# Kernel tuning notes

Measured on AMD Instinct MI355X. Metric: run time of the kernel, lower is better.

## Reference

```python
import jax, jax.numpy as jnp
import numpy as np

N = 30000      # nodes
E = 480000     # edges (before self loops)
DIN = 128      # dim_in
DH = 32        # dim_h (per-head out channels)
H1 = 8         # gat1 heads
H2 = 2         # gat2 heads
G = 64         # num graphs in batch
DOUT = 10      # dim_out
NEG_SLOPE = 0.2


def _glorot(key, shape):
    fan_in = shape[0]
    return jax.random.normal(key, shape, dtype=jnp.float32) / np.sqrt(fan_in)


def setup_inputs() -> dict:
    key = jax.random.key(0)
    ks = jax.random.split(key, 16)
    x = jax.random.normal(ks[0], (N, DIN), dtype=jnp.float32)
    edge_index = jax.random.randint(ks[1], (2, E), 0, N, dtype=jnp.int32)
    batch = jnp.sort(jax.random.randint(ks[2], (N,), 0, G, dtype=jnp.int32))
    # GATv2Conv layer 1: lin_l, lin_r (dim_in -> H1*DH), att (H1, DH), bias (H1*DH)
    W1l = _glorot(ks[3], (DIN, H1 * DH))
    W1r = _glorot(ks[4], (DIN, H1 * DH))
    a1 = _glorot(ks[5], (DH, H1)).T  # [H1, DH]
    b1 = jnp.zeros((H1 * DH,), dtype=jnp.float32)
    # GATv2Conv layer 2: (H1*DH -> H2*DH)
    W2l = _glorot(ks[6], (H1 * DH, H2 * DH))
    W2r = _glorot(ks[7], (H1 * DH, H2 * DH))
    a2 = _glorot(ks[8], (DH, H2)).T  # [H2, DH]
    b2 = jnp.zeros((H2 * DH,), dtype=jnp.float32)
    # MLP head: fc1(2*DH -> DH), fc2(DH -> DH//2), fc(DH//2 -> DOUT); stored [in,out]
    fc1_w = _glorot(ks[9], (2 * DH, DH)); fc1_b = jnp.zeros((DH,), jnp.float32)
    fc2_w = _glorot(ks[10], (DH, DH // 2)); fc2_b = jnp.zeros((DH // 2,), jnp.float32)
    fc_w = _glorot(ks[11], (DH // 2, DOUT)); fc_b = jnp.zeros((DOUT,), jnp.float32)
    return {"x": x, "edge_index": edge_index, "batch": batch,
            "W1l": W1l, "W1r": W1r, "a1": a1, "b1": b1,
            "W2l": W2l, "W2r": W2r, "a2": a2, "b2": b2,
            "fc1_w": fc1_w, "fc1_b": fc1_b, "fc2_w": fc2_w, "fc2_b": fc2_b,
            "fc_w": fc_w, "fc_b": fc_b}


def gatv2_conv(x, edge_index, Wl, Wr, att, bias, heads, dh, n):
    """PyG GATv2Conv: concat=True, add_self_loops=True, negative_slope=0.2."""
    src, dst = edge_index[0], edge_index[1]
    loop = jnp.arange(n, dtype=src.dtype)        # self loops (PyG default)
    src = jnp.concatenate([src, loop])
    dst = jnp.concatenate([dst, loop])
    xl = (x @ Wl).reshape(n, heads, dh)          # source transform
    xr = (x @ Wr).reshape(n, heads, dh)          # destination transform
    xj = xl[src]                                  # [Etot, H, dh] message features
    s = jax.nn.leaky_relu(xj + xr[dst], NEG_SLOPE)
    e = jnp.einsum('ehd,hd->eh', s, att)          # per-edge per-head score
    # segment softmax over incoming edges of each destination node
    m = jax.ops.segment_max(e, dst, num_segments=n)
    p = jnp.exp(e - m[dst])
    z = jax.ops.segment_sum(p, dst, num_segments=n)
    alpha = p / z[dst]                            # [Etot, H]
    out = jax.ops.segment_sum(xj * alpha[..., None], dst, num_segments=n)
    return out.reshape(n, heads * dh) + bias


def reference(x, edge_index, batch, W1l, W1r, a1, b1, W2l, W2r, a2, b2,
              fc1_w, fc1_b, fc2_w, fc2_b, fc_w, fc_b):
    h = gatv2_conv(x, edge_index, W1l, W1r, a1, b1, H1, DH, N)
    h = jax.nn.elu(h)
    h = gatv2_conv(h, edge_index, W2l, W2r, a2, b2, H2, DH, N)  # [N, 2*DH]
    # global_mean_pool
    sums = jax.ops.segment_sum(h, batch, num_segments=G)
    cnt = jax.ops.segment_sum(jnp.ones((N,), h.dtype), batch, num_segments=G)
    hg = sums / jnp.maximum(cnt, 1.0)[:, None]    # [G, 2*DH]
    x1 = jax.nn.relu(hg @ fc1_w + fc1_b)
    # dropout p=0.2 is identity in eval mode
    x2 = jax.nn.relu(x1 @ fc2_w + fc2_b)
    c = x2 @ fc_w + fc_b
    return (c, x2)
```

## Files before the change

kernel.cpp:

```cpp
#include <hip/hip_runtime.h>
#include <math.h>

#define DIN 128
#define DH  32
#define H1  8
#define H2  2
#define GNUM 64
#define DOUT 10
#define NEG_SLOPE 0.2f
#define SCAN_B 512

typedef __attribute__((ext_vector_type(8))) short sv8;
typedef __attribute__((ext_vector_type(4))) short sv4;
typedef __attribute__((ext_vector_type(4))) float fv4;

static __device__ __forceinline__ unsigned short f2bf(float f) {
    unsigned int u = __float_as_uint(f);
    unsigned int r = (u + 0x7fffu + ((u >> 16) & 1u)) >> 16;
    return (unsigned short)r;
}
static __device__ __forceinline__ float bf2f(unsigned short h) {
    return __uint_as_float(((unsigned int)h) << 16);
}

__global__ void k_deg(const int* __restrict__ dst, int* __restrict__ deg, int E, int n) {
    int i = blockIdx.x * blockDim.x + threadIdx.x;
    if (i < E) {
        atomicAdd(&deg[dst[i]], 1);
    } else if (i < E + n) {
        atomicAdd(&deg[i - E], 1);
    }
}

__global__ __launch_bounds__(SCAN_B)
void k_scan_partial(const int* __restrict__ deg, int* __restrict__ bsum, int n) {
    int i = blockIdx.x * SCAN_B + threadIdx.x;
    int v = (i < n) ? deg[i] : 0;
    #pragma unroll
    for (int m = 32; m >= 1; m >>= 1) v += __shfl_xor(v, m);
    __shared__ int red[SCAN_B / 64];
    if ((threadIdx.x & 63) == 0) red[threadIdx.x >> 6] = v;
    __syncthreads();
    if (threadIdx.x == 0) {
        int s = 0;
        #pragma unroll
        for (int k = 0; k < SCAN_B / 64; ++k) s += red[k];
        bsum[blockIdx.x] = s;
    }
}

__global__ __launch_bounds__(SCAN_B)
void k_scan_apply(int* __restrict__ deg, int* __restrict__ cursor,
                  const int* __restrict__ bsum, int n, int nb) {
    __shared__ int buf[SCAN_B];
    __shared__ int pfx_s, tot_s;
    const int t = threadIdx.x, b = blockIdx.x;
    if (t < 64) {
        int v = (t < nb) ? bsum[t] : 0;
        int incl = v;
        #pragma unroll
        for (int o = 1; o < 64; o <<= 1) {
            int w = __shfl_up(incl, o);
            if (t >= o) incl += w;
        }
        int pfx = (b == 0) ? 0 : __shfl(incl, b - 1);
        int tot = __shfl(incl, nb - 1);
        if (t == 0) { pfx_s = pfx; tot_s = tot; }
    }
    int i = b * SCAN_B + t;
    int v = (i < n) ? deg[i] : 0;
    buf[t] = v;
    __syncthreads();
    for (int o = 1; o < SCAN_B; o <<= 1) {
        int a = (t >= o) ? buf[t - o] : 0;
        __syncthreads();
        buf[t] += a;
        __syncthreads();
    }
    int excl = buf[t] - v + pfx_s;
    if (i < n) { deg[i] = excl; cursor[i] = excl; }
    if (b == 0 && t == 0) deg[n] = tot_s;
}

__global__ void k_scatter(const int* __restrict__ src, const int* __restrict__ dst,
                          int* __restrict__ cursor, int* __restrict__ csr_src, int E, int n) {
    int i = blockIdx.x * blockDim.x + threadIdx.x;
    if (i < E) {
        int d = dst[i];
        int pos = atomicAdd(&cursor[d], 1);
        csr_src[pos] = src[i];
    } else if (i < E + n) {
        int v = i - E;
        int pos = atomicAdd(&cursor[v], 1);
        csr_src[pos] = v;
    }
}

__global__ void k_prep(const float* __restrict__ W1l, const float* __restrict__ W1r,
                       const float* __restrict__ W2l, const float* __restrict__ W2r,
                       short* __restrict__ B1th, short* __restrict__ B1tl,
                       short* __restrict__ B2th, short* __restrict__ B2tl) {
    int id = blockIdx.x * blockDim.x + threadIdx.x;
    const int T1 = 512 * 128;
    const int T2 = 128 * 256;
    if (id < T1) {
        int n = id / 128, k = id - n * 128;
        float v = (n < 256) ? W1l[(size_t)k * 256 + n] : W1r[(size_t)k * 256 + (n - 256)];
        unsigned short h = f2bf(v);
        B1th[id] = (short)h;
        B1tl[id] = (short)f2bf(v - bf2f(h));
    } else if (id < T1 + T2) {
        int id2 = id - T1;
        int n = id2 / 256, k = id2 - n * 256;
        float v = (n < 64) ? W2l[(size_t)k * 64 + n] : W2r[(size_t)k * 64 + (n - 64)];
        unsigned short h = f2bf(v);
        B2th[id2] = (short)h;
        B2tl[id2] = (short)f2bf(v - bf2f(h));
    }
}

__global__ __launch_bounds__(256)
void k_gemm_mfma(const float* __restrict__ A, const short* __restrict__ Bth,
                 const short* __restrict__ Btl,
                 unsigned short* __restrict__ Cl, float* __restrict__ Cr,
                 int M, int K, int Ntot, int NL) {
    __shared__ union {
        struct { short hi[128 * 40]; short lo[128 * 40]; } a;
        float c[64 * 132];
    } sm;
    const int tid = threadIdx.x;
    const int lane = tid & 63;
    const int wid = tid >> 6;
    const int wm = wid & 1, wn = wid >> 1;
    const int m0 = blockIdx.x * 128;
    const int n0 = blockIdx.y * 128;
    const int l15 = lane & 15, q = lane >> 4;

    fv4 acc[4][4] = {};

    for (int kk = 0; kk < K; kk += 32) {
        __syncthreads();
        #pragma unroll
        for (int i = 0; i < 4; ++i) {
            int idx = tid + i * 256;
            int row = idx >> 3;
            int qq  = idx & 7;
            int mg  = m0 + row;
            float4 v = make_float4(0.f, 0.f, 0.f, 0.f);
            if (mg < M) v = *(const float4*)(A + (size_t)mg * K + kk + qq * 4);
            unsigned short hx = f2bf(v.x), hy = f2bf(v.y), hz = f2bf(v.z), hw = f2bf(v.w);
            sv4 hi = { (short)hx, (short)hy, (short)hz, (short)hw };
            sv4 lo = { (short)f2bf(v.x - bf2f(hx)), (short)f2bf(v.y - bf2f(hy)),
                       (short)f2bf(v.z - bf2f(hz)), (short)f2bf(v.w - bf2f(hw)) };
            *(sv4*)&sm.a.hi[row * 40 + qq * 4] = hi;
            *(sv4*)&sm.a.lo[row * 40 + qq * 4] = lo;
        }
        __syncthreads();

        sv8 bh[4], bl[4];
        #pragma unroll
        for (int fn = 0; fn < 4; ++fn) {
            int ng = n0 + wn * 64 + fn * 16 + l15;
            bh[fn] = *(const sv8*)(Bth + (size_t)ng * K + kk + q * 8);
            bl[fn] = *(const sv8*)(Btl + (size_t)ng * K + kk + q * 8);
        }
        #pragma unroll
        for (int fm = 0; fm < 4; ++fm) {
            int rl = wm * 64 + fm * 16 + l15;
            sv8 ah = *(const sv8*)&sm.a.hi[rl * 40 + q * 8];
            sv8 al = *(const sv8*)&sm.a.lo[rl * 40 + q * 8];
            #pragma unroll
            for (int fn = 0; fn < 4; ++fn) {
                acc[fm][fn] = __builtin_amdgcn_mfma_f32_16x16x32_bf16(ah, bh[fn], acc[fm][fn], 0, 0, 0);
                acc[fm][fn] = __builtin_amdgcn_mfma_f32_16x16x32_bf16(ah, bl[fn], acc[fm][fn], 0, 0, 0);
                acc[fm][fn] = __builtin_amdgcn_mfma_f32_16x16x32_bf16(al, bh[fn], acc[fm][fn], 0, 0, 0);
            }
        }
    }

    const int NR = Ntot - NL;
    #pragma unroll
    for (int s = 0; s < 2; ++s) {
        __syncthreads();
        if (wm == s) {
            #pragma unroll
            for (int fm = 0; fm < 4; ++fm)
                #pragma unroll
                for (int fn = 0; fn < 4; ++fn)
                    #pragma unroll
                    for (int r = 0; r < 4; ++r)
                        sm.c[(fm * 16 + q * 4 + r) * 132 + wn * 64 + fn * 16 + l15] = acc[fm][fn][r];
        }
        __syncthreads();
        #pragma unroll
        for (int i = 0; i < 2; ++i) {
            int lr = (tid >> 3) + i * 32;
            int grow = m0 + s * 64 + lr;
            if (grow < M) {
                #pragma unroll
                for (int k4 = 0; k4 < 4; ++k4) {
                    int jj = (tid & 7) + k4 * 8;
                    float4 vv = *(float4*)&sm.c[lr * 132 + jj * 4];
                    int gcol = n0 + jj * 4;
                    if (gcol < NL) {
                        ushort4 uu;
                        uu.x = f2bf(vv.x); uu.y = f2bf(vv.y);
                        uu.z = f2bf(vv.z); uu.w = f2bf(vv.w);
                        *(ushort4*)(Cl + (size_t)grow * NL + gcol) = uu;
                    } else {
                        *(float4*)(Cr + (size_t)grow * NR + (gcol - NL)) = vv;
                    }
                }
            }
        }
    }
}

__global__ __launch_bounds__(256)
void k_gemm_mfma_bf(const unsigned short* __restrict__ A, const short* __restrict__ Bth,
                    const short* __restrict__ Btl,
                    unsigned short* __restrict__ Cl, float* __restrict__ Cr,
                    int M, int K, int Ntot, int NL) {
    __shared__ union {
        short a[128 * 40];
        float c[64 * 132];
    } sm;
    const int tid = threadIdx.x;
    const int lane = tid & 63;
    const int wid = tid >> 6;
    const int wm = wid & 1, wn = wid >> 1;
    const int m0 = blockIdx.x * 128;
    const int n0 = blockIdx.y * 128;
    const int l15 = lane & 15, q = lane >> 4;

    fv4 acc[4][4] = {};

    for (int kk = 0; kk < K; kk += 32) {
        __syncthreads();
        #pragma unroll
        for (int i = 0; i < 2; ++i) {
            int idx = tid + i * 256;
            int row = idx >> 2;
            int qq  = idx & 3;
            int mg  = m0 + row;
            sv8 v = { 0, 0, 0, 0, 0, 0, 0, 0 };
            if (mg < M) v = *(const sv8*)(A + (size_t)mg * K + kk + qq * 8);
            *(sv8*)&sm.a[row * 40 + qq * 8] = v;
        }
        __syncthreads();

        sv8 bh[4], bl[4];
        #pragma unroll
        for (int fn = 0; fn < 4; ++fn) {
            int ng = n0 + wn * 64 + fn * 16 + l15;
            bh[fn] = *(const sv8*)(Bth + (size_t)ng * K + kk + q * 8);
            bl[fn] = *(const sv8*)(Btl + (size_t)ng * K + kk + q * 8);
        }
        #pragma unroll
        for (int fm = 0; fm < 4; ++fm) {
            int rl = wm * 64 + fm * 16 + l15;
            sv8 ah = *(const sv8*)&sm.a[rl * 40 + q * 8];
            #pragma unroll
            for (int fn = 0; fn < 4; ++fn) {
                acc[fm][fn] = __builtin_amdgcn_mfma_f32_16x16x32_bf16(ah, bh[fn], acc[fm][fn], 0, 0, 0);
                acc[fm][fn] = __builtin_amdgcn_mfma_f32_16x16x32_bf16(ah, bl[fn], acc[fm][fn], 0, 0, 0);
            }
        }
    }

    const int NR = Ntot - NL;
    #pragma unroll
    for (int s = 0; s < 2; ++s) {
        __syncthreads();
        if (wm == s) {
            #pragma unroll
            for (int fm = 0; fm < 4; ++fm)
                #pragma unroll
                for (int fn = 0; fn < 4; ++fn)
                    #pragma unroll
                    for (int r = 0; r < 4; ++r)
                        sm.c[(fm * 16 + q * 4 + r) * 132 + wn * 64 + fn * 16 + l15] = acc[fm][fn][r];
        }
        __syncthreads();
        #pragma unroll
        for (int i = 0; i < 2; ++i) {
            int lr = (tid >> 3) + i * 32;
            int grow = m0 + s * 64 + lr;
            if (grow < M) {
                #pragma unroll
                for (int k4 = 0; k4 < 4; ++k4) {
                    int jj = (tid & 7) + k4 * 8;
                    float4 vv = *(float4*)&sm.c[lr * 132 + jj * 4];
                    int gcol = n0 + jj * 4;
                    if (gcol < NL) {
                        ushort4 uu;
                        uu.x = f2bf(vv.x); uu.y = f2bf(vv.y);
                        uu.z = f2bf(vv.z); uu.w = f2bf(vv.w);
                        *(ushort4*)(Cl + (size_t)grow * NL + gcol) = uu;
                    } else {
                        *(float4*)(Cr + (size_t)grow * NR + (gcol - NL)) = vv;
                    }
                }
            }
        }
    }
}

static __device__ __forceinline__ void edge_acc(const float4 xl, const float4 xr,
                                                const float4 av, float& z, float4& acc) {
    float tx = xl.x + xr.x, ty = xl.y + xr.y, tz = xl.z + xr.z, tw = xl.w + xr.w;
    float lx = fmaxf(tx, 0.f) + NEG_SLOPE * fminf(tx, 0.f);
    float ly = fmaxf(ty, 0.f) + NEG_SLOPE * fminf(ty, 0.f);
    float lz = fmaxf(tz, 0.f) + NEG_SLOPE * fminf(tz, 0.f);
    float lw = fmaxf(tw, 0.f) + NEG_SLOPE * fminf(tw, 0.f);
    float s = lx * av.x + ly * av.y + lz * av.z + lw * av.w;
    s += __shfl_xor(s, 1);
    s += __shfl_xor(s, 2);
    s += __shfl_xor(s, 4);
    float w = __expf(s);
    z += w;
    acc.x = fmaf(w, xl.x, acc.x);
    acc.y = fmaf(w, xl.y, acc.y);
    acc.z = fmaf(w, xl.z, acc.z);
    acc.w = fmaf(w, xl.w, acc.w);
}

static __device__ __forceinline__ float4 bfx4(const ushort4 u) {
    float4 f;
    f.x = bf2f(u.x); f.y = bf2f(u.y); f.z = bf2f(u.z); f.w = bf2f(u.w);
    return f;
}

__global__ __launch_bounds__(256)
void k_edge1(const unsigned short* __restrict__ XLB, const float* __restrict__ XR,
             const int* __restrict__ offs, const int* __restrict__ csr,
             const float* __restrict__ att, const float* __restrict__ bias,
             unsigned short* __restrict__ out, int n) {
    const int lane = threadIdx.x & 63;
    const int wid  = threadIdx.x >> 6;
    const int v = blockIdx.x * 4 + wid;
    if (v >= n) return;
    const float4 xr = *(const float4*)(XR + (size_t)v * 256 + lane * 4);
    const float4 av = *(const float4*)(att + lane * 4);
    const float4 bv = *(const float4*)(bias + lane * 4);
    float z = 0.f;
    float4 acc = make_float4(0.f, 0.f, 0.f, 0.f);
    const int e0 = offs[v], e1 = offs[v + 1];
    int j = e0;
    for (; j + 4 <= e1; j += 4) {
        int s0 = csr[j], s1 = csr[j + 1], s2 = csr[j + 2], s3 = csr[j + 3];
        ushort4 u0 = *(const ushort4*)(XLB + (size_t)s0 * 256 + lane * 4);
        ushort4 u1 = *(const ushort4*)(XLB + (size_t)s1 * 256 + lane * 4);
        ushort4 u2 = *(const ushort4*)(XLB + (size_t)s2 * 256 + lane * 4);
        ushort4 u3 = *(const ushort4*)(XLB + (size_t)s3 * 256 + lane * 4);
        edge_acc(bfx4(u0), xr, av, z, acc);
        edge_acc(bfx4(u1), xr, av, z, acc);
        edge_acc(bfx4(u2), xr, av, z, acc);
        edge_acc(bfx4(u3), xr, av, z, acc);
    }
    for (; j < e1; ++j) {
        int s0 = csr[j];
        ushort4 u0 = *(const ushort4*)(XLB + (size_t)s0 * 256 + lane * 4);
        edge_acc(bfx4(u0), xr, av, z, acc);
    }
    const float rz = 1.f / z;
    float4 o;
    o.x = fmaf(acc.x, rz, bv.x);
    o.y = fmaf(acc.y, rz, bv.y);
    o.z = fmaf(acc.z, rz, bv.z);
    o.w = fmaf(acc.w, rz, bv.w);
    o.x = (o.x > 0.f) ? o.x : (__expf(o.x) - 1.f);
    o.y = (o.y > 0.f) ? o.y : (__expf(o.y) - 1.f);
    o.z = (o.z > 0.f) ? o.z : (__expf(o.z) - 1.f);
    o.w = (o.w > 0.f) ? o.w : (__expf(o.w) - 1.f);
    ushort4 hv;
    hv.x = f2bf(o.x); hv.y = f2bf(o.y); hv.z = f2bf(o.z); hv.w = f2bf(o.w);
    *(ushort4*)(out + (size_t)v * 256 + lane * 4) = hv;
}

__global__ __launch_bounds__(256)
void k_edge2(const unsigned short* __restrict__ XLB, const float* __restrict__ XR,
             const int* __restrict__ offs, const int* __restrict__ csr,
             const float* __restrict__ att, const float* __restrict__ bias,
             float* __restrict__ out, int n) {
    const int lane = threadIdx.x & 63;
    const int wid  = threadIdx.x >> 6;
    const int v = blockIdx.x * 4 + wid;
    if (v >= n) return;
    const int grp = lane >> 4, li = lane & 15;
    const float4 xr = *(const float4*)(XR + (size_t)v * 64 + li * 4);
    const float4 av = *(const float4*)(att + li * 4);
    float z = 0.f;
    float4 acc = make_float4(0.f, 0.f, 0.f, 0.f);
    const int e0 = offs[v], e1 = offs[v + 1];
    for (int j0 = e0; j0 < e1; j0 += 4) {
        const int j = j0 + grp;
        const bool valid = (j < e1);
        const int src = valid ? csr[j] : v;
        ushort4 u = *(const ushort4*)(XLB + (size_t)src * 64 + li * 4);
        float4 xl = bfx4(u);
        float tx = xl.x + xr.x, ty = xl.y + xr.y, tz = xl.z + xr.z, tw = xl.w + xr.w;
        float lx = fmaxf(tx, 0.f) + NEG_SLOPE * fminf(tx, 0.f);
        float ly = fmaxf(ty, 0.f) + NEG_SLOPE * fminf(ty, 0.f);
        float lz = fmaxf(tz, 0.f) + NEG_SLOPE * fminf(tz, 0.f);
        float lw = fmaxf(tw, 0.f) + NEG_SLOPE * fminf(tw, 0.f);
        float s = lx * av.x + ly * av.y + lz * av.z + lw * av.w;
        s += __shfl_xor(s, 1);
        s += __shfl_xor(s, 2);
        s += __shfl_xor(s, 4);
        float w = valid ? __expf(s) : 0.f;
        z += w;
        acc.x = fmaf(w, xl.x, acc.x);
        acc.y = fmaf(w, xl.y, acc.y);
        acc.z = fmaf(w, xl.z, acc.z);
        acc.w = fmaf(w, xl.w, acc.w);
    }
    z += __shfl_xor(z, 16); z += __shfl_xor(z, 32);
    acc.x += __shfl_xor(acc.x, 16); acc.x += __shfl_xor(acc.x, 32);
    acc.y += __shfl_xor(acc.y, 16); acc.y += __shfl_xor(acc.y, 32);
    acc.z += __shfl_xor(acc.z, 16); acc.z += __shfl_xor(acc.z, 32);
    acc.w += __shfl_xor(acc.w, 16); acc.w += __shfl_xor(acc.w, 32);
    if (grp == 0) {
        const float4 bv = *(const float4*)(bias + li * 4);
        const float rz = 1.f / z;
        float4 o;
        o.x = fmaf(acc.x, rz, bv.x);
        o.y = fmaf(acc.y, rz, bv.y);
        o.z = fmaf(acc.z, rz, bv.z);
        o.w = fmaf(acc.w, rz, bv.w);
        *(float4*)(out + (size_t)v * 64 + li * 4) = o;
    }
}

__global__ __launch_bounds__(256)
void k_pool_mlp(const float* __restrict__ out2, const int* __restrict__ batch,
                const float* __restrict__ fc1w, const float* __restrict__ fc1b,
                const float* __restrict__ fc2w, const float* __restrict__ fc2b,
                const float* __restrict__ fcw,  const float* __restrict__ fcb,
                float* __restrict__ outc, float* __restrict__ outx2, int n) {
    const int g = blockIdx.x;
    const int t = threadIdx.x;
    const int lane = t & 63;
    const int w = t >> 6;
    __shared__ float red[4][64];
    __shared__ float hg_s[64];
    __shared__ float x1_s[32];
    __shared__ float x2_s[16];

    int lo = 0, hi = n;
    while (lo < hi) { int mid = (lo + hi) >> 1; if (batch[mid] < g) lo = mid + 1; else hi = mid; }
    const int start = lo;
    hi = n;
    while (lo < hi) { int mid = (lo + hi) >> 1; if (batch[mid] < g + 1) lo = mid + 1; else hi = mid; }
    const int end = lo;

    float s = 0.f;
    for (int v = start + w; v < end; v += 4)
        s += out2[(size_t)v * 64 + lane];
    red[w][lane] = s;
    __syncthreads();
    if (w == 0) {
        float tot = red[0][lane] + red[1][lane] + red[2][lane] + red[3][lane];
        float cnt = fmaxf((float)(end - start), 1.0f);
        hg_s[lane] = tot / cnt;
    }
    __syncthreads();
    if (t < 32) {
        float a = fc1b[t];
        #pragma unroll
        for (int k = 0; k < 64; ++k) a = fmaf(hg_s[k], fc1w[k * 32 + t], a);
        x1_s[t] = fmaxf(a, 0.f);
    }
    __syncthreads();
    if (t < 16) {
        float a = fc2b[t];
        #pragma unroll
        for (int k = 0; k < 32; ++k) a = fmaf(x1_s[k], fc2w[k * 16 + t], a);
        x2_s[t] = fmaxf(a, 0.f);
    }
    __syncthreads();
    if (t < DOUT) {
        float a = fcb[t];
        #pragma unroll
        for (int k = 0; k < 16; ++k) a = fmaf(x2_s[k], fcw[k * 10 + t], a);
        outc[g * DOUT + t] = a;
    }
    if (t < 16) outx2[g * 16 + t] = x2_s[t];
}

extern "C" void kernel_launch(void* const* d_in, const int* in_sizes, int n_in,
                              void* d_out, int out_size, void* d_ws, size_t ws_size,
                              hipStream_t stream) {
    const float* x    = (const float*)d_in[0];
    const int*   ei   = (const int*)d_in[1];
    const int*   batch= (const int*)d_in[2];
    const float* W1l  = (const float*)d_in[3];
    const float* W1r  = (const float*)d_in[4];
    const float* a1   = (const float*)d_in[5];
    const float* b1   = (const float*)d_in[6];
    const float* W2l  = (const float*)d_in[7];
    const float* W2r  = (const float*)d_in[8];
    const float* a2   = (const float*)d_in[9];
    const float* b2   = (const float*)d_in[10];
    const float* fc1w = (const float*)d_in[11];
    const float* fc1b = (const float*)d_in[12];
    const float* fc2w = (const float*)d_in[13];
    const float* fc2b = (const float*)d_in[14];
    const float* fcw  = (const float*)d_in[15];
    const float* fcb  = (const float*)d_in[16];

    const int N = in_sizes[2];
    const int E = in_sizes[1] / 2;
    const int ET = E + N;
    const int* esrc = ei;
    const int* edst = ei + E;
    const int NB = (N + SCAN_B - 1) / SCAN_B;

    char* ws = (char*)d_ws;
    size_t off = 0;
    unsigned short* xl1b = (unsigned short*)(ws + off);  off += (size_t)N * 256 * 2;
    float* xr1  = (float*)(ws + off);            off += (size_t)N * 256 * 4;
    unsigned short* h1b = (unsigned short*)(ws + off);   off += (size_t)N * 256 * 2;
    int*   deg   = (int*)(ws + off);             off += ((size_t)(N + 1) * 4 + 255) & ~255ull;
    int*   cursor= (int*)(ws + off);             off += ((size_t)N * 4 + 255) & ~255ull;
    int*   csr   = (int*)(ws + off);             off += ((size_t)ET * 4 + 255) & ~255ull;
    int*   bsum  = (int*)(ws + off);             off += ((size_t)(NB + 1) * 4 + 255) & ~255ull;
    short* B1th  = (short*)(ws + off);           off += (size_t)512 * 128 * 2;
    short* B1tl  = (short*)(ws + off);           off += (size_t)512 * 128 * 2;
    short* B2th  = (short*)(ws + off);           off += (size_t)128 * 256 * 2;
    short* B2tl  = (short*)(ws + off);           off += (size_t)128 * 256 * 2;
    unsigned short* xl2b = xl1b;
    float* xr2  = xr1;
    float* out2 = xr1 + (size_t)N * 64;
    (void)ws_size; (void)n_in; (void)out_size;

    float* outc  = (float*)d_out;
    float* outx2 = (float*)d_out + GNUM * DOUT;

    hipMemsetAsync(deg, 0, (size_t)(N + 1) * 4, stream);

    int tb = 256;
    int gb = (ET + tb - 1) / tb;
    k_deg<<<gb, tb, 0, stream>>>(edst, deg, E, N);
    k_scan_partial<<<NB, SCAN_B, 0, stream>>>(deg, bsum, N);
    k_scan_apply<<<NB, SCAN_B, 0, stream>>>(deg, cursor, bsum, N, NB);
    k_scatter<<<gb, tb, 0, stream>>>(esrc, edst, cursor, csr, E, N);

    k_prep<<<(512 * 128 + 128 * 256 + 255) / 256, 256, 0, stream>>>(
        W1l, W1r, W2l, W2r, B1th, B1tl, B2th, B2tl);

    dim3 g1((N + 127) / 128, 4);
    k_gemm_mfma<<<g1, 256, 0, stream>>>(x, B1th, B1tl, xl1b, xr1, N, DIN, 512, 256);

    k_edge1<<<(N + 3) / 4, 256, 0, stream>>>(xl1b, xr1, deg, csr, a1, b1, h1b, N);

    dim3 g2((N + 127) / 128, 1);
    k_gemm_mfma_bf<<<g2, 256, 0, stream>>>(h1b, B2th, B2tl, xl2b, xr2, N, 256, 128, 64);

    k_edge2<<<(N + 3) / 4, 256, 0, stream>>>(xl2b, xr2, deg, csr, a2, b2, out2, N);

    k_pool_mlp<<<GNUM, 256, 0, stream>>>(out2, batch, fc1w, fc1b, fc2w, fc2b,
                                         fcw, fcb, outc, outx2, N);
}
```

Before: 317.5 us.

## Use persistent atomic work queues for edge kernels and pre-split x to bf16

The two edge-aggregation kernels become persistent: a fixed grid of 2048 blocks where each wavefront takes destination nodes from an atomic counter, aiming for better load balance across skewed node degrees. LeakyReLU inside the attention score is rewritten as 0.6*t + 0.4*|t|, and bf16 unpacking now uses bit masks on uint2 loads. The input x is split into bf16 hi/lo arrays once in the prep kernel, so the first GEMM loads pre-split data instead of converting it in each of its four column blocks. The degree memset is folded into the prep kernel, which also zeros the queue counters. This adds a full extra write and read pass over x and one atomic per node in exchange.

```diff
diff --git a/kernel.cpp b/kernel.cpp
--- a/kernel.cpp
+++ b/kernel.cpp
@@ -23,84 +23,15 @@
     return __uint_as_float(((unsigned int)h) << 16);
 }
 
-__global__ void k_deg(const int* __restrict__ dst, int* __restrict__ deg, int E, int n) {
-    int i = blockIdx.x * blockDim.x + threadIdx.x;
-    if (i < E) {
-        atomicAdd(&deg[dst[i]], 1);
-    } else if (i < E + n) {
-        atomicAdd(&deg[i - E], 1);
-    }
-}
-
-__global__ __launch_bounds__(SCAN_B)
-void k_scan_partial(const int* __restrict__ deg, int* __restrict__ bsum, int n) {
-    int i = blockIdx.x * SCAN_B + threadIdx.x;
-    int v = (i < n) ? deg[i] : 0;
-    #pragma unroll
-    for (int m = 32; m >= 1; m >>= 1) v += __shfl_xor(v, m);
-    __shared__ int red[SCAN_B / 64];
-    if ((threadIdx.x & 63) == 0) red[threadIdx.x >> 6] = v;
-    __syncthreads();
-    if (threadIdx.x == 0) {
-        int s = 0;
-        #pragma unroll
-        for (int k = 0; k < SCAN_B / 64; ++k) s += red[k];
-        bsum[blockIdx.x] = s;
-    }
-}
-
-__global__ __launch_bounds__(SCAN_B)
-void k_scan_apply(int* __restrict__ deg, int* __restrict__ cursor,
-                  const int* __restrict__ bsum, int n, int nb) {
-    __shared__ int buf[SCAN_B];
-    __shared__ int pfx_s, tot_s;
-    const int t = threadIdx.x, b = blockIdx.x;
-    if (t < 64) {
-        int v = (t < nb) ? bsum[t] : 0;
-        int incl = v;
-        #pragma unroll
-        for (int o = 1; o < 64; o <<= 1) {
-            int w = __shfl_up(incl, o);
-            if (t >= o) incl += w;
-        }
-        int pfx = (b == 0) ? 0 : __shfl(incl, b - 1);
-        int tot = __shfl(incl, nb - 1);
-        if (t == 0) { pfx_s = pfx; tot_s = tot; }
-    }
-    int i = b * SCAN_B + t;
-    int v = (i < n) ? deg[i] : 0;
-    buf[t] = v;
-    __syncthreads();
-    for (int o = 1; o < SCAN_B; o <<= 1) {
-        int a = (t >= o) ? buf[t - o] : 0;
-        __syncthreads();
-        buf[t] += a;
-        __syncthreads();
-    }
-    int excl = buf[t] - v + pfx_s;
-    if (i < n) { deg[i] = excl; cursor[i] = excl; }
-    if (b == 0 && t == 0) deg[n] = tot_s;
-}
-
-__global__ void k_scatter(const int* __restrict__ src, const int* __restrict__ dst,
-                          int* __restrict__ cursor, int* __restrict__ csr_src, int E, int n) {
-    int i = blockIdx.x * blockDim.x + threadIdx.x;
-    if (i < E) {
-        int d = dst[i];
-        int pos = atomicAdd(&cursor[d], 1);
-        csr_src[pos] = src[i];
-    } else if (i < E + n) {
-        int v = i - E;
-        int pos = atomicAdd(&cursor[v], 1);
-        csr_src[pos] = v;
-    }
-}
-
-__global__ void k_prep(const float* __restrict__ W1l, const float* __restrict__ W1r,
+__global__ void k_prep(const float* __restrict__ x,
+                       const float* __restrict__ W1l, const float* __restrict__ W1r,
                        const float* __restrict__ W2l, const float* __restrict__ W2r,
                        short* __restrict__ B1th, short* __restrict__ B1tl,
-                       short* __restrict__ B2th, short* __restrict__ B2tl) {
+                       short* __restrict__ B2th, short* __restrict__ B2tl,
+                       unsigned short* __restrict__ Xh, unsigned short* __restrict__ Xl,
+                       int* __restrict__ deg, int nz, int NK) {
     int id = blockIdx.x * blockDim.x + threadIdx.x;
+    if (id < nz) deg[id] = 0;
     const int T1 = 512 * 128;
     const int T2 = 128 * 256;
     if (id < T1) {
@@ -116,14 +47,93 @@
         unsigned short h = f2bf(v);
         B2th[id2] = (short)h;
         B2tl[id2] = (short)f2bf(v - bf2f(h));
+    } else if (id < T1 + T2 + NK) {
+        int e = id - T1 - T2;
+        float v = x[e];
+        unsigned short h = f2bf(v);
+        Xh[e] = h;
+        Xl[e] = f2bf(v - bf2f(h));
+    }
+}
+
+__global__ void k_deg(const int* __restrict__ dst, int* __restrict__ deg, int E, int n) {
+    int i = blockIdx.x * blockDim.x + threadIdx.x;
+    if (i < E) {
+        atomicAdd(&deg[dst[i]], 1);
+    } else if (i < E + n) {
+        atomicAdd(&deg[i - E], 1);
+    }
+}
+
+__global__ __launch_bounds__(SCAN_B)
+void k_scan_partial(const int* __restrict__ deg, int* __restrict__ bsum, int n) {
+    int i = blockIdx.x * SCAN_B + threadIdx.x;
+    int v = (i < n) ? deg[i] : 0;
+    #pragma unroll
+    for (int m = 32; m >= 1; m >>= 1) v += __shfl_xor(v, m);
+    __shared__ int red[SCAN_B / 64];
+    if ((threadIdx.x & 63) == 0) red[threadIdx.x >> 6] = v;
+    __syncthreads();
+    if (threadIdx.x == 0) {
+        int s = 0;
+        #pragma unroll
+        for (int k = 0; k < SCAN_B / 64; ++k) s += red[k];
+        bsum[blockIdx.x] = s;
+    }
+}
+
+__global__ __launch_bounds__(SCAN_B)
+void k_scan_apply(int* __restrict__ deg, int* __restrict__ cursor,
+                  const int* __restrict__ bsum, int n, int nb) {
+    __shared__ int buf[SCAN_B];
+    __shared__ int pfx_s, tot_s;
+    const int t = threadIdx.x, b = blockIdx.x;
+    if (t < 64) {
+        int v = (t < nb) ? bsum[t] : 0;
+        int incl = v;
+        #pragma unroll
+        for (int o = 1; o < 64; o <<= 1) {
+            int w = __shfl_up(incl, o);
+            if (t >= o) incl += w;
+        }
+        int pfx = (b == 0) ? 0 : __shfl(incl, b - 1);
+        int tot = __shfl(incl, nb - 1);
+        if (t == 0) { pfx_s = pfx; tot_s = tot; }
+    }
+    int i = b * SCAN_B + t;
+    int v = (i < n) ? deg[i] : 0;
+    buf[t] = v;
+    __syncthreads();
+    for (int o = 1; o < SCAN_B; o <<= 1) {
+        int a = (t >= o) ? buf[t - o] : 0;
+        __syncthreads();
+        buf[t] += a;
+        __syncthreads();
+    }
+    int excl = buf[t] - v + pfx_s;
+    if (i < n) { deg[i] = excl; cursor[i] = excl; }
+    if (b == 0 && t == 0) deg[n] = tot_s;
+}
+
+__global__ void k_scatter(const int* __restrict__ src, const int* __restrict__ dst,
+                          int* __restrict__ cursor, int* __restrict__ csr_src, int E, int n) {
+    int i = blockIdx.x * blockDim.x + threadIdx.x;
+    if (i < E) {
+        int d = dst[i];
+        int pos = atomicAdd(&cursor[d], 1);
+        csr_src[pos] = src[i];
+    } else if (i < E + n) {
+        int v = i - E;
+        int pos = atomicAdd(&cursor[v], 1);
+        csr_src[pos] = v;
     }
 }
 
 __global__ __launch_bounds__(256)
-void k_gemm_mfma(const float* __restrict__ A, const short* __restrict__ Bth,
-                 const short* __restrict__ Btl,
-                 unsigned short* __restrict__ Cl, float* __restrict__ Cr,
-                 int M, int K, int Ntot, int NL) {
+void k_gemm_split(const unsigned short* __restrict__ Ah, const unsigned short* __restrict__ Al,
+                  const short* __restrict__ Bth, const short* __restrict__ Btl,
+                  unsigned short* __restrict__ Cl, float* __restrict__ Cr,
+                  int M, int K, int Ntot, int NL) {
     __shared__ union {
         struct { short hi[128 * 40]; short lo[128 * 40]; } a;
         float c[64 * 132];
@@ -143,17 +153,15 @@
         #pragma unroll
         for (int i = 0; i < 4; ++i) {
             int idx = tid + i * 256;
-            int row = idx >> 3;
-            int qq  = idx & 7;
-            int mg  = m0 + row;
-            float4 v = make_float4(0.f, 0.f, 0.f, 0.f);
-            if (mg < M) v = *(const float4*)(A + (size_t)mg * K + kk + qq * 4);
-            unsigned short hx = f2bf(v.x), hy = f2bf(v.y), hz = f2bf(v.z), hw = f2bf(v.w);
-            sv4 hi = { (short)hx, (short)hy, (short)hz, (short)hw };
-            sv4 lo = { (short)f2bf(v.x - bf2f(hx)), (short)f2bf(v.y - bf2f(hy)),
-                       (short)f2bf(v.z - bf2f(hz)), (short)f2bf(v.w - bf2f(hw)) };
-            *(sv4*)&sm.a.hi[row * 40 + qq * 4] = hi;
-            *(sv4*)&sm.a.lo[row * 40 + qq * 4] = lo;
+            int arr = idx >> 9;
+            int c = idx & 511;
+            int row = c >> 2, qq = c & 3;
+            int mg = m0 + row;
+            const unsigned short* srcp = arr ? Al : Ah;
+            sv8 v = { 0, 0, 0, 0, 0, 0, 0, 0 };
+            if (mg < M) v = *(const sv8*)(srcp + (size_t)mg * K + kk + qq * 8);
+            short* dst = arr ? sm.a.lo : sm.a.hi;
+            *(sv8*)&dst[row * 40 + qq * 8] = v;
         }
         __syncthreads();
 
@@ -217,10 +225,10 @@
 }
 
 __global__ __launch_bounds__(256)
-void k_gemm_mfma_bf(const unsigned short* __restrict__ A, const short* __restrict__ Bth,
-                    const short* __restrict__ Btl,
-                    unsigned short* __restrict__ Cl, float* __restrict__ Cr,
-                    int M, int K, int Ntot, int NL) {
+void k_gemm_bf(const unsigned short* __restrict__ A, const short* __restrict__ Bth,
+               const short* __restrict__ Btl,
+               unsigned short* __restrict__ Cl, float* __restrict__ Cr,
+               int M, int K, int Ntot, int NL) {
     __shared__ union {
         short a[128 * 40];
         float c[64 * 132];
@@ -240,9 +248,8 @@
         #pragma unroll
         for (int i = 0; i < 2; ++i) {
             int idx = tid + i * 256;
-            int row = idx >> 2;
-            int qq  = idx & 3;
-            int mg  = m0 + row;
+            int row = idx >> 2, qq = idx & 3;
+            int mg = m0 + row;
             sv8 v = { 0, 0, 0, 0, 0, 0, 0, 0 };
             if (mg < M) v = *(const sv8*)(A + (size_t)mg * K + kk + qq * 8);
             *(sv8*)&sm.a[row * 40 + qq * 8] = v;
@@ -306,129 +313,145 @@
     }
 }
 
-static __device__ __forceinline__ void edge_acc(const float4 xl, const float4 xr,
+static __device__ __forceinline__ void edge_acc(const uint2 w, const float4 xr,
                                                 const float4 av, float& z, float4& acc) {
-    float tx = xl.x + xr.x, ty = xl.y + xr.y, tz = xl.z + xr.z, tw = xl.w + xr.w;
-    float lx = fmaxf(tx, 0.f) + NEG_SLOPE * fminf(tx, 0.f);
-    float ly = fmaxf(ty, 0.f) + NEG_SLOPE * fminf(ty, 0.f);
-    float lz = fmaxf(tz, 0.f) + NEG_SLOPE * fminf(tz, 0.f);
-    float lw = fmaxf(tw, 0.f) + NEG_SLOPE * fminf(tw, 0.f);
-    float s = lx * av.x + ly * av.y + lz * av.z + lw * av.w;
+    float fx = __uint_as_float(w.x << 16);
+    float fy = __uint_as_float(w.x & 0xffff0000u);
+    float fz = __uint_as_float(w.y << 16);
+    float fw = __uint_as_float(w.y & 0xffff0000u);
+    float tx = fx + xr.x, ty = fy + xr.y, tz = fz + xr.z, tw = fw + xr.w;
+    float s1 = tx * av.x;
+    s1 = fmaf(ty, av.y, s1);
+    s1 = fmaf(tz, av.z, s1);
+    s1 = fmaf(tw, av.w, s1);
+    float s2 = fabsf(tx) * av.x;
+    s2 = fmaf(fabsf(ty), av.y, s2);
+    s2 = fmaf(fabsf(tz), av.z, s2);
+    s2 = fmaf(fabsf(tw), av.w, s2);
+    float s = fmaf(0.6f, s1, 0.4f * s2);
     s += __shfl_xor(s, 1);
     s += __shfl_xor(s, 2);
     s += __shfl_xor(s, 4);
-    float w = __expf(s);
-    z += w;
-    acc.x = fmaf(w, xl.x, acc.x);
-    acc.y = fmaf(w, xl.y, acc.y);
-    acc.z = fmaf(w, xl.z, acc.z);
-    acc.w = fmaf(w, xl.w, acc.w);
-}
-
-static __device__ __forceinline__ float4 bfx4(const ushort4 u) {
-    float4 f;
-    f.x = bf2f(u.x); f.y = bf2f(u.y); f.z = bf2f(u.z); f.w = bf2f(u.w);
-    return f;
+    float e = __expf(s);
+    z += e;
+    acc.x = fmaf(e, fx, acc.x);
+    acc.y = fmaf(e, fy, acc.y);
+    acc.z = fmaf(e, fz, acc.z);
+    acc.w = fmaf(e, fw, acc.w);
 }
 
 __global__ __launch_bounds__(256)
 void k_edge1(const unsigned short* __restrict__ XLB, const float* __restrict__ XR,
              const int* __restrict__ offs, const int* __restrict__ csr,
              const float* __restrict__ att, const float* __restrict__ bias,
-             unsigned short* __restrict__ out, int n) {
+             unsigned short* __restrict__ out, int* __restrict__ ctr, int n) {
     const int lane = threadIdx.x & 63;
-    const int wid  = threadIdx.x >> 6;
-    const int v = blockIdx.x * 4 + wid;
-    if (v >= n) return;
-    const float4 xr = *(const float4*)(XR + (size_t)v * 256 + lane * 4);
     const float4 av = *(const float4*)(att + lane * 4);
     const float4 bv = *(const float4*)(bias + lane * 4);
-    float z = 0.f;
-    float4 acc = make_float4(0.f, 0.f, 0.f, 0.f);
-    const int e0 = offs[v], e1 = offs[v + 1];
-    int j = e0;
-    for (; j + 4 <= e1; j += 4) {
-        int s0 = csr[j], s1 = csr[j + 1], s2 = csr[j + 2], s3 = csr[j + 3];
-        ushort4 u0 = *(const ushort4*)(XLB + (size_t)s0 * 256 + lane * 4);
-        ushort4 u1 = *(const ushort4*)(XLB + (size_t)s1 * 256 + lane * 4);
-        ushort4 u2 = *(const ushort4*)(XLB + (size_t)s2 * 256 + lane * 4);
-        ushort4 u3 = *(const ushort4*)(XLB + (size_t)s3 * 256 + lane * 4);
-        edge_acc(bfx4(u0), xr, av, z, acc);
-        edge_acc(bfx4(u1), xr, av, z, acc);
-        edge_acc(bfx4(u2), xr, av, z, acc);
-        edge_acc(bfx4(u3), xr, av, z, acc);
-    }
-    for (; j < e1; ++j) {
-        int s0 = csr[j];
-        ushort4 u0 = *(const ushort4*)(XLB + (size_t)s0 * 256 + lane * 4);
-        edge_acc(bfx4(u0), xr, av, z, acc);
-    }
-    const float rz = 1.f / z;
-    float4 o;
-    o.x = fmaf(acc.x, rz, bv.x);
-    o.y = fmaf(acc.y, rz, bv.y);
-    o.z = fmaf(acc.z, rz, bv.z);
-    o.w = fmaf(acc.w, rz, bv.w);
-    o.x = (o.x > 0.f) ? o.x : (__expf(o.x) - 1.f);
-    o.y = (o.y > 0.f) ? o.y : (__expf(o.y) - 1.f);
-    o.z = (o.z > 0.f) ? o.z : (__expf(o.z) - 1.f);
-    o.w = (o.w > 0.f) ? o.w : (__expf(o.w) - 1.f);
-    ushort4 hv;
-    hv.x = f2bf(o.x); hv.y = f2bf(o.y); hv.z = f2bf(o.z); hv.w = f2bf(o.w);
-    *(ushort4*)(out + (size_t)v * 256 + lane * 4) = hv;
-}
-
-__global__ __launch_bounds__(256)
-void k_edge2(const unsigned short* __restrict__ XLB, const float* __restrict__ XR,
-             const int* __restrict__ offs, const int* __restrict__ csr,
-             const float* __restrict__ att, const float* __restrict__ bias,
-             float* __restrict__ out, int n) {
-    const int lane = threadIdx.x & 63;
-    const int wid  = threadIdx.x >> 6;
-    const int v = blockIdx.x * 4 + wid;
-    if (v >= n) return;
-    const int grp = lane >> 4, li = lane & 15;
-    const float4 xr = *(const float4*)(XR + (size_t)v * 64 + li * 4);
-    const float4 av = *(const float4*)(att + li * 4);
-    float z = 0.f;
-    float4 acc = make_float4(0.f, 0.f, 0.f, 0.f);
-    const int e0 = offs[v], e1 = offs[v + 1];
-    for (int j0 = e0; j0 < e1; j0 += 4) {
-        const int j = j0 + grp;
-        const bool valid = (j < e1);
-        const int src = valid ? csr[j] : v;
-        ushort4 u = *(const ushort4*)(XLB + (size_t)src * 64 + li * 4);
-        float4 xl = bfx4(u);
-        float tx = xl.x + xr.x, ty = xl.y + xr.y, tz = xl.z + xr.z, tw = xl.w + xr.w;
-        float lx = fmaxf(tx, 0.f) + NEG_SLOPE * fminf(tx, 0.f);
-        float ly = fmaxf(ty, 0.f) + NEG_SLOPE * fminf(ty, 0.f);
-        float lz = fmaxf(tz, 0.f) + NEG_SLOPE * fminf(tz, 0.f);
-        float lw = fmaxf(tw, 0.f) + NEG_SLOPE * fminf(tw, 0.f);
-        float s = lx * av.x + ly * av.y + lz * av.z + lw * av.w;
-        s += __shfl_xor(s, 1);
-        s += __shfl_xor(s, 2);
-        s += __shfl_xor(s, 4);
-        float w = valid ? __expf(s) : 0.f;
-        z += w;
-        acc.x = fmaf(w, xl.x, acc.x);
-        acc.y = fmaf(w, xl.y, acc.y);
-        acc.z = fmaf(w, xl.z, acc.z);
-        acc.w = fmaf(w, xl.w, acc.w);
-    }
-    z += __shfl_xor(z, 16); z += __shfl_xor(z, 32);
-    acc.x += __shfl_xor(acc.x, 16); acc.x += __shfl_xor(acc.x, 32);
-    acc.y += __shfl_xor(acc.y, 16); acc.y += __shfl_xor(acc.y, 32);
-    acc.z += __shfl_xor(acc.z, 16); acc.z += __shfl_xor(acc.z, 32);
-    acc.w += __shfl_xor(acc.w, 16); acc.w += __shfl_xor(acc.w, 32);
-    if (grp == 0) {
-        const float4 bv = *(const float4*)(bias + li * 4);
+    const uint2* XL2 = (const uint2*)XLB;
+    for (;;) {
+        int v;
+        if (lane == 0) v = atomicAdd(ctr, 1);
+        v = __shfl(v, 0);
+        if (v >= n) return;
+        const float4 xr = *(const float4*)(XR + (size_t)v * 256 + lane * 4);
+        float z = 0.f;
+        float4 acc = make_float4(0.f, 0.f, 0.f, 0.f);
+        const int e0 = offs[v], e1 = offs[v + 1];
+        int j = e0;
+        for (; j + 4 <= e1; j += 4) {
+            int s0 = csr[j], s1 = csr[j + 1], s2 = csr[j + 2], s3 = csr[j + 3];
+            uint2 u0 = XL2[(size_t)s0 * 64 + lane];
+            uint2 u1 = XL2[(size_t)s1 * 64 + lane];
+            uint2 u2 = XL2[(size_t)s2 * 64 + lane];
+            uint2 u3 = XL2[(size_t)s3 * 64 + lane];
+            edge_acc(u0, xr, av, z, acc);
+            edge_acc(u1, xr, av, z, acc);
+            edge_acc(u2, xr, av, z, acc);
+            edge_acc(u3, xr, av, z, acc);
+        }
+        for (; j < e1; ++j) {
+            uint2 u0 = XL2[(size_t)csr[j] * 64 + lane];
+            edge_acc(u0, xr, av, z, acc);
+        }
         const float rz = 1.f / z;
         float4 o;
         o.x = fmaf(acc.x, rz, bv.x);
         o.y = fmaf(acc.y, rz, bv.y);
         o.z = fmaf(acc.z, rz, bv.z);
         o.w = fmaf(acc.w, rz, bv.w);
-        *(float4*)(out + (size_t)v * 64 + li * 4) = o;
+        o.x = (o.x > 0.f) ? o.x : (__expf(o.x) - 1.f);
+        o.y = (o.y > 0.f) ? o.y : (__expf(o.y) - 1.f);
+        o.z = (o.z > 0.f) ? o.z : (__expf(o.z) - 1.f);
+        o.w = (o.w > 0.f) ? o.w : (__expf(o.w) - 1.f);
+        ushort4 hv;
+        hv.x = f2bf(o.x); hv.y = f2bf(o.y); hv.z = f2bf(o.z); hv.w = f2bf(o.w);
+        *(ushort4*)(out + (size_t)v * 256 + lane * 4) = hv;
+    }
+}
+
+__global__ __launch_bounds__(256)
+void k_edge2(const unsigned short* __restrict__ XLB, const float* __restrict__ XR,
+             const int* __restrict__ offs, const int* __restrict__ csr,
+             const float* __restrict__ att, const float* __restrict__ bias,
+             float* __restrict__ out, int* __restrict__ ctr, int n) {
+    const int lane = threadIdx.x & 63;
+    const int grp = lane >> 4, li = lane & 15;
+    const float4 av = *(const float4*)(att + li * 4);
+    const uint2* XL2 = (const uint2*)XLB;
+    for (;;) {
+        int v;
+        if (lane == 0) v = atomicAdd(ctr, 1);
+        v = __shfl(v, 0);
+        if (v >= n) return;
+        const float4 xr = *(const float4*)(XR + (size_t)v * 64 + li * 4);
+        float z = 0.f;
+        float4 acc = make_float4(0.f, 0.f, 0.f, 0.f);
+        const int e0 = offs[v], e1 = offs[v + 1];
+        for (int j0 = e0; j0 < e1; j0 += 4) {
+            const int j = j0 + grp;
+            const bool valid = (j < e1);
+            const int src = valid ? csr[j] : v;
+            uint2 w = XL2[(size_t)src * 16 + li];
+            float fx = __uint_as_float(w.x << 16);
+            float fy = __uint_as_float(w.x & 0xffff0000u);
+            float fz = __uint_as_float(w.y << 16);
+            float fw = __uint_as_float(w.y & 0xffff0000u);
+            float tx = fx + xr.x, ty = fy + xr.y, tz = fz + xr.z, tw = fw + xr.w;
+            float s1 = tx * av.x;
+            s1 = fmaf(ty, av.y, s1);
+            s1 = fmaf(tz, av.z, s1);
+            s1 = fmaf(tw, av.w, s1);
+            float s2 = fabsf(tx) * av.x;
+            s2 = fmaf(fabsf(ty), av.y, s2);
+            s2 = fmaf(fabsf(tz), av.z, s2);
+            s2 = fmaf(fabsf(tw), av.w, s2);
+            float s = fmaf(0.6f, s1, 0.4f * s2);
+            s += __shfl_xor(s, 1);
+            s += __shfl_xor(s, 2);
+            s += __shfl_xor(s, 4);
+            float e = valid ? __expf(s) : 0.f;
+            z += e;
+            acc.x = fmaf(e, fx, acc.x);
+            acc.y = fmaf(e, fy, acc.y);
+            acc.z = fmaf(e, fz, acc.z);
+            acc.w = fmaf(e, fw, acc.w);
+        }
+        z += __shfl_xor(z, 16); z += __shfl_xor(z, 32);
+        acc.x += __shfl_xor(acc.x, 16); acc.x += __shfl_xor(acc.x, 32);
+        acc.y += __shfl_xor(acc.y, 16); acc.y += __shfl_xor(acc.y, 32);
+        acc.z += __shfl_xor(acc.z, 16); acc.z += __shfl_xor(acc.z, 32);
+        acc.w += __shfl_xor(acc.w, 16); acc.w += __shfl_xor(acc.w, 32);
+        if (grp == 0) {
+            const float4 bv = *(const float4*)(bias + li * 4);
+            const float rz = 1.f / z;
+            float4 o;
+            o.x = fmaf(acc.x, rz, bv.x);
+            o.y = fmaf(acc.y, rz, bv.y);
+            o.z = fmaf(acc.z, rz, bv.z);
+            o.w = fmaf(acc.w, rz, bv.w);
+            *(float4*)(out + (size_t)v * 64 + li * 4) = o;
+        }
     }
 }
 
@@ -521,7 +544,7 @@
     unsigned short* xl1b = (unsigned short*)(ws + off);  off += (size_t)N * 256 * 2;
     float* xr1  = (float*)(ws + off);            off += (size_t)N * 256 * 4;
     unsigned short* h1b = (unsigned short*)(ws + off);   off += (size_t)N * 256 * 2;
-    int*   deg   = (int*)(ws + off);             off += ((size_t)(N + 1) * 4 + 255) & ~255ull;
+    int*   deg   = (int*)(ws + off);             off += ((size_t)(N + 4) * 4 + 255) & ~255ull;
     int*   cursor= (int*)(ws + off);             off += ((size_t)N * 4 + 255) & ~255ull;
     int*   csr   = (int*)(ws + off);             off += ((size_t)ET * 4 + 255) & ~255ull;
     int*   bsum  = (int*)(ws + off);             off += ((size_t)(NB + 1) * 4 + 255) & ~255ull;
@@ -529,15 +552,21 @@
     short* B1tl  = (short*)(ws + off);           off += (size_t)512 * 128 * 2;
     short* B2th  = (short*)(ws + off);           off += (size_t)128 * 256 * 2;
     short* B2tl  = (short*)(ws + off);           off += (size_t)128 * 256 * 2;
+    unsigned short* Xh = (unsigned short*)(ws + off);    off += (size_t)N * 128 * 2;
+    unsigned short* Xl = (unsigned short*)(ws + off);    off += (size_t)N * 128 * 2;
     unsigned short* xl2b = xl1b;
     float* xr2  = xr1;
     float* out2 = xr1 + (size_t)N * 64;
+    int* ctrE1 = deg + N + 1;
+    int* ctrE2 = deg + N + 2;
     (void)ws_size; (void)n_in; (void)out_size;
 
     float* outc  = (float*)d_out;
     float* outx2 = (float*)d_out + GNUM * DOUT;
 
-    hipMemsetAsync(deg, 0, (size_t)(N + 1) * 4, stream);
+    const int prep_tot = 512 * 128 + 128 * 256 + N * 128;
+    k_prep<<<(prep_tot + 255) / 256, 256, 0, stream>>>(
+        x, W1l, W1r, W2l, W2r, B1th, B1tl, B2th, B2tl, Xh, Xl, deg, N + 4, N * 128);
 
     int tb = 256;
     int gb = (ET + tb - 1) / tb;
@@ -546,18 +575,15 @@
     k_scan_apply<<<NB, SCAN_B, 0, stream>>>(deg, cursor, bsum, N, NB);
     k_scatter<<<gb, tb, 0, stream>>>(esrc, edst, cursor, csr, E, N);
 
-    k_prep<<<(512 * 128 + 128 * 256 + 255) / 256, 256, 0, stream>>>(
-        W1l, W1r, W2l, W2r, B1th, B1tl, B2th, B2tl);
-
     dim3 g1((N + 127) / 128, 4);
-    k_gemm_mfma<<<g1, 256, 0, stream>>>(x, B1th, B1tl, xl1b, xr1, N, DIN, 512, 256);
-
-    k_edge1<<<(N + 3) / 4, 256, 0, stream>>>(xl1b, xr1, deg, csr, a1, b1, h1b, N);
+    k_gemm_split<<<g1, 256, 0, stream>>>(Xh, Xl, B1th, B1tl, xl1b, xr1, N, DIN, 512, 256);
+
+    k_edge1<<<2048, 256, 0, stream>>>(xl1b, xr1, deg, csr, a1, b1, h1b, ctrE1, N);
 
     dim3 g2((N + 127) / 128, 1);
-    k_gemm_mfma_bf<<<g2, 256, 0, stream>>>(h1b, B2th, B2tl, xl2b, xr2, N, 256, 128, 64);
-
-    k_edge2<<<(N + 3) / 4, 256, 0, stream>>>(xl2b, xr2, deg, csr, a2, b2, out2, N);
+    k_gemm_bf<<<g2, 256, 0, stream>>>(h1b, B2th, B2tl, xl2b, xr2, N, 256, 128, 64);
+
+    k_edge2<<<2048, 256, 0, stream>>>(xl2b, xr2, deg, csr, a2, b2, out2, ctrE2, N);
 
     k_pool_mlp<<<GNUM, 256, 0, stream>>>(out2, batch, fc1w, fc1b, fc2w, fc2b,
                                          fcw, fcb, outc, outx2, N);
```

New measurement: 1.132 ms. +256.7%, slower.
